# Kernel tuning notes

Hardware: AMD Instinct MI355X
Metric: run time of the kernel (lower is better)

## Reference

```python
import jax, jax.numpy as jnp
import numpy as np

NUM_QUBITS = 21
NUM_LAYERS = 4
ACTION_DIM = 18
STATE_DIM = 2 ** NUM_QUBITS  # amplitude register size


def _rx(t):
    c = jnp.cos(t / 2)
    s = jnp.sin(t / 2)
    return jnp.stack([jnp.stack([c + 0j, -1j * s]), jnp.stack([-1j * s, c + 0j])]).astype(jnp.complex64)


def _ry(t):
    c = jnp.cos(t / 2)
    s = jnp.sin(t / 2)
    return jnp.stack([jnp.stack([c, -s]), jnp.stack([s, c])]).astype(jnp.complex64)


def _rz(t):
    e = jnp.exp(-1j * t / 2).astype(jnp.complex64)
    z = jnp.zeros_like(e)
    return jnp.stack([jnp.stack([e, z]), jnp.stack([z, jnp.conj(e)])])


def apply_1q(psi, U, q):
    # wire 0 is the most-significant bit (PennyLane convention)
    s = psi.reshape(2 ** q, 2, -1)
    s = jnp.einsum('ab,xbz->xaz', U, s)
    return s.reshape(-1)


def apply_cnot(psi, c, t):
    a, b = (c, t) if c < t else (t, c)
    s = psi.reshape(2 ** a, 2, 2 ** (b - a - 1), 2, -1)
    ctrl_ax = 1 if c < t else 3
    tgt_ax = 3 if c < t else 1
    s0 = jax.lax.index_in_dim(s, 0, axis=ctrl_ax, keepdims=False)
    s1 = jax.lax.index_in_dim(s, 1, axis=ctrl_ax, keepdims=False)
    tgt_in_slab = tgt_ax if tgt_ax < ctrl_ax else tgt_ax - 1
    s1 = jnp.flip(s1, axis=tgt_in_slab)  # X on target where control==1
    s = jnp.stack([s0, s1], axis=ctrl_ax)
    return s.reshape(-1)


def _layer(psi, lp, entangle):
    # lp: (NUM_QUBITS, 3) rotation angles for this layer
    for q in range(NUM_QUBITS):
        psi = apply_1q(psi, _rx(lp[q, 0]), q)
        psi = apply_1q(psi, _ry(lp[q, 1]), q)
        psi = apply_1q(psi, _rz(lp[q, 2]), q)
    if entangle:
        for q in range(NUM_QUBITS - 1):
            psi = apply_cnot(psi, q, q + 1)
        psi = apply_cnot(psi, NUM_QUBITS - 1, 0)
    return psi


def setup_inputs() -> dict:
    key = jax.random.key(0)
    k1, k2, k3, k4 = jax.random.split(key, 4)
    state = jax.random.normal(k1, (STATE_DIM,), dtype=jnp.float32)
    circuit_params = jax.random.normal(k2, (NUM_LAYERS * NUM_QUBITS * 3,), dtype=jnp.float32) * 0.01
    bound = 1.0 / np.sqrt(NUM_QUBITS)
    head_w = jax.random.uniform(k3, (ACTION_DIM, NUM_QUBITS), jnp.float32, -bound, bound)
    head_b = jax.random.uniform(k4, (ACTION_DIM,), jnp.float32, -bound, bound)
    return {'state': state, 'circuit_params': circuit_params, 'head_w': head_w, 'head_b': head_b}


def reference(state, circuit_params, head_w, head_b):
    # Amplitude encoding: normalize (state_dim == 2**num_qubits so no padding needed)
    norm = jnp.linalg.norm(state)
    inv = jnp.where(norm > 0, 1.0 / jnp.maximum(norm, 1e-30), 0.0)
    basis0 = jnp.zeros((STATE_DIM,), jnp.float32).at[0].set(1.0)
    amp = jnp.where(norm > 0, state * inv, basis0)
    psi = amp.astype(jnp.complex64)

    lp = circuit_params.reshape(NUM_LAYERS, NUM_QUBITS, 3)
    for layer in range(NUM_LAYERS):
        psi = _layer(psi, lp[layer], layer < NUM_LAYERS - 1)

    # Pauli-Z expectation values per qubit from |psi|^2
    probs = psi.real ** 2 + psi.imag ** 2
    zvals = []
    for q in range(NUM_QUBITS):
        p = probs.reshape(2 ** q, 2, -1)
        zvals.append(p[:, 0, :].sum() - p[:, 1, :].sum())
    meas = jnp.stack(zvals).astype(jnp.float32)

    logits = head_w @ meas + head_b
    return jax.nn.softmax(logits, axis=-1)
```

## Files before the change

### kernel.cpp

```cpp
#include <hip/hip_runtime.h>

#define NQ 21
#define DIM (1 << NQ)
#define NL 4
#define ADIM 18
#define GB 512
#define NT 512

__device__ __forceinline__ float2 cfma2(float2 u0, float2 a, float2 u1, float2 b) {
    return make_float2(u0.x * a.x - u0.y * a.y + u1.x * b.x - u1.y * b.y,
                       u0.x * a.y + u0.y * a.x + u1.x * b.y + u1.y * b.x);
}

struct GateU { float2 u00, u01, u10, u11; };

__device__ __forceinline__ void bfly(float2& a, float2& b, const GateU& U) {
    float2 na = cfma2(U.u00, a, U.u01, b);
    float2 nb = cfma2(U.u10, a, U.u11, b);
    a = na; b = nb;
}

__device__ __forceinline__ int sw(int j) { return j ^ (((j >> 4) & 7) << 1); }

__device__ __forceinline__ void make_mats(GateU* mats, const float* __restrict__ cp, int layer, int tid) {
    if (tid < NQ) {
        const float* ang = cp + (layer * NQ + tid) * 3;
        float a = ang[0], b = ang[1], c = ang[2];
        float ca = cosf(0.5f * a), sa = sinf(0.5f * a);
        float cb = cosf(0.5f * b), sb = sinf(0.5f * b);
        float cc = cosf(0.5f * c), sc = sinf(0.5f * c);
        float2 m00 = make_float2(cb * ca,  sb * sa);
        float2 m01 = make_float2(-sb * ca, -cb * sa);
        float2 m10 = make_float2(sb * ca,  -cb * sa);
        float2 m11 = make_float2(cb * ca,  -sb * sa);
        GateU U;
        U.u00 = make_float2(cc * m00.x + sc * m00.y, cc * m00.y - sc * m00.x);
        U.u01 = make_float2(cc * m01.x + sc * m01.y, cc * m01.y - sc * m01.x);
        U.u10 = make_float2(cc * m10.x - sc * m10.y, cc * m10.y + sc * m10.x);
        U.u11 = make_float2(cc * m11.x - sc * m11.y, cc * m11.y + sc * m11.x);
        mats[tid] = U;
    }
}

__device__ __forceinline__ void round3(float2* tile, int tid, int g,
                                       GateU Ua, GateU Ub, GateU Uc) {
    int bl = (1 << g) - 1;
    int base = (tid & bl) | ((tid >> g) << (g + 3));
    float2 v[8];
#pragma unroll
    for (int j = 0; j < 8; ++j) v[j] = tile[sw(base + (j << g))];
#pragma unroll
    for (int s = 0; s < 8; s += 2) bfly(v[s], v[s + 1], Ua);
#pragma unroll
    for (int s = 0; s < 8; ++s) if (!(s & 2)) bfly(v[s], v[s | 2], Ub);
#pragma unroll
    for (int s = 0; s < 8; ++s) if (!(s & 4)) bfly(v[s], v[s | 4], Uc);
#pragma unroll
    for (int j = 0; j < 8; ++j) tile[sw(base + (j << g))] = v[j];
    __syncthreads();
}

__global__ __launch_bounds__(NT, 4) void k_passB(const float* __restrict__ state,
                                                 float2* __restrict__ psi,
                                                 const float* __restrict__ cp, int layer) {
    __shared__ float2 tile[4096];
    __shared__ GateU mats[NQ];
    const int tid = threadIdx.x, blk = blockIdx.x;
    float4* psi4 = (float4*)psi;
    float4* t4 = (float4*)tile;

    if (layer == 0) {
        const float4* s4 = (const float4*)state;
        for (int it = 0; it < 2; ++it) {
            int f2 = it * NT + tid;
            int h = f2 >> 1, c2 = f2 & 1;
            float4 w = s4[(h << 10) | (blk << 1) | c2];
            int j = 8 * h + 4 * c2;
            t4[sw(j) >> 1]     = make_float4(w.x, 0.f, w.y, 0.f);
            t4[sw(j + 2) >> 1] = make_float4(w.z, 0.f, w.w, 0.f);
        }
        make_mats(mats, cp, layer, tid);
        __syncthreads();
        round3(tile, tid, 3, mats[8], mats[7], mats[6]);
        round3(tile, tid, 6, mats[5], mats[4], mats[3]);
        round3(tile, tid, 9, mats[2], mats[1], mats[0]);
    } else {
        float2 v[8];
        float4 w[4];
        for (int i = 0; i < 4; ++i) {
            int f = i * NT + tid;
            int h = f >> 2, c = f & 3;
            w[i] = psi4[(h << 11) | (blk << 2) | c];
        }
        make_mats(mats, cp, layer, tid);
        __syncthreads();
#pragma unroll
        for (int i = 0; i < 4; ++i) {
            v[2 * i]     = make_float2(w[i].x, w[i].y);
            v[2 * i + 1] = make_float2(w[i ^ 2].z, w[i ^ 2].w);
        }
        GateU U0 = mats[0];
#pragma unroll
        for (int s = 0; s < 8; ++s) if (!(s & 4)) bfly(v[s], v[s | 4], U0);
        GateU U1 = mats[1];
#pragma unroll
        for (int s = 0; s < 8; ++s) if (!(s & 2)) bfly(v[s], v[s | 2], U1);
        for (int i = 0; i < 4; ++i)
            t4[sw(2 * (i * NT + tid)) >> 1] =
                make_float4(v[2 * i].x, v[2 * i].y, v[2 * i + 1].x, v[2 * i + 1].y);
        __syncthreads();
        round3(tile, tid, 3, mats[8], mats[7], mats[6]);
        round3(tile, tid, 6, mats[5], mats[4], mats[3]);
        {
            GateU U = mats[2];
            for (int it = 0; it < 4; ++it) {
                int p = it * NT + tid;
                int i0 = ((p >> 9) << 10) | (p & 511);
                bfly(tile[sw(i0)], tile[sw(i0 | 512)], U);
            }
            __syncthreads();
        }
    }
    int srcmask = (layer < 3) ? 0xFF : 0;
    for (int i = 0; i < 4; ++i) {
        int f = i * NT + tid;
        int h = f >> 2, c = f & 3;
        int hs = h ^ ((h >> 1) & srcmask);
        int j = sw(hs * 8 + 2 * c);
        float2 e0 = tile[j], e1 = tile[j + 1];
        psi4[(h << 11) | (blk << 2) | c] = make_float4(e0.x, e0.y, e1.x, e1.y);
    }
}

__global__ __launch_bounds__(NT, 4) void k_passA(float2* __restrict__ psi,
                                                 const float* __restrict__ cp, int layer,
                                                 float* __restrict__ partials) {
    __shared__ float2 tile[4096];
    __shared__ GateU mats[NQ];
    const int tid = threadIdx.x, blk = blockIdx.x;
    float4* psi4 = (float4*)psi;
    float4* t4 = (float4*)tile;

    {
        const float4* ga = psi4 + (size_t)blk * 2048;
        float2 v[8];
        float4 w[4];
        for (int i = 0; i < 4; ++i) w[i] = ga[i * NT + tid];
        make_mats(mats, cp, layer, tid);
        __syncthreads();
#pragma unroll
        for (int i = 0; i < 4; ++i) {
            v[2 * i]     = make_float2(w[i].x, w[i].y);
            v[2 * i + 1] = make_float2(w[i].z, w[i].w);
        }
        GateU U20 = mats[20];
#pragma unroll
        for (int s = 0; s < 8; s += 2) bfly(v[s], v[s + 1], U20);
        GateU U10 = mats[10];
#pragma unroll
        for (int s = 0; s < 8; ++s) if (!(s & 2)) bfly(v[s], v[s | 2], U10);
        GateU U9 = mats[9];
#pragma unroll
        for (int s = 0; s < 8; ++s) if (!(s & 4)) bfly(v[s], v[s | 4], U9);
        for (int i = 0; i < 4; ++i)
            t4[sw(2 * (i * NT + tid)) >> 1] =
                make_float4(v[2 * i].x, v[2 * i].y, v[2 * i + 1].x, v[2 * i + 1].y);
    }
    __syncthreads();
    round3(tile, tid, 1, mats[19], mats[18], mats[17]);
    round3(tile, tid, 4, mats[16], mats[15], mats[14]);
    round3(tile, tid, 7, mats[13], mats[12], mats[11]);

    if (layer < 3) {
        float4* oa = psi4 + (size_t)blk * 2048;
        int cb = (blk & 1) << 11;
        for (int i = 0; i < 4; ++i) {
            int f = i * NT + tid;
            int s0 = ((2 * f) ^ (f & 0x7FF)) ^ cb;
            float2 e0 = tile[sw(s0)], e1 = tile[sw(s0 ^ 1)];
            oa[f] = make_float4(e0.x, e0.y, e1.x, e1.y);
        }
    } else {
        float tot = 0.f, ones[NQ];
#pragma unroll
        for (int q = 0; q < NQ; ++q) ones[q] = 0.f;
        for (int it = 0; it < 8; ++it) {
            int j = it * NT + tid;
            float2 a2 = tile[sw(j)];
            float pr = a2.x * a2.x + a2.y * a2.y;
            int gidx = (blk << 12) | j;
            tot += pr;
#pragma unroll
            for (int q = 0; q < NQ; ++q)
                ones[q] += pr * (float)((gidx >> (20 - q)) & 1);
        }
        for (int off = 32; off; off >>= 1) {
            tot += __shfl_down(tot, off, 64);
#pragma unroll
            for (int q = 0; q < NQ; ++q) ones[q] += __shfl_down(ones[q], off, 64);
        }
        __syncthreads();
        float* red = (float*)tile;
        int wv = tid >> 6, ln = tid & 63;
        if (ln == 0) {
            red[wv * 22 + 21] = tot;
#pragma unroll
            for (int q = 0; q < NQ; ++q) red[wv * 22 + q] = ones[q];
        }
        __syncthreads();
        if (tid < 22) {
            float s = 0.f;
            for (int wvi = 0; wvi < 8; ++wvi) s += red[wvi * 22 + tid];
            partials[blk * 22 + tid] = s;
        }
    }
}

__global__ __launch_bounds__(NT) void k_final(const float* __restrict__ partials,
                                              const float* __restrict__ head_w,
                                              const float* __restrict__ head_b,
                                              float* __restrict__ out) {
    __shared__ float red[640];
    __shared__ float meas[NQ];
    __shared__ float lg[ADIM];
    int tid = threadIdx.x;
    int col = tid % 22, grp = tid / 22;
    if (tid < 506) {
        float s = 0.f;
        for (int r = grp; r < GB; r += 23) s += partials[r * 22 + col];
        red[grp * 22 + col] = s;
    }
    __syncthreads();
    if (tid < 22) {
        float t2 = 0.f;
        for (int g = 0; g < 23; ++g) t2 += red[g * 22 + tid];
        red[600 + tid] = t2;
    }
    __syncthreads();
    if (tid < NQ) {
        float tot = red[600 + 21];
        meas[tid] = (tot > 0.f) ? (1.f - 2.f * red[600 + tid] / tot) : 1.f;
    }
    __syncthreads();
    if (tid < ADIM) {
        float s2 = head_b[tid];
        for (int q = 0; q < NQ; ++q) s2 += head_w[tid * NQ + q] * meas[q];
        lg[tid] = s2;
    }
    __syncthreads();
    if (tid == 0) {
        float m = lg[0];
        for (int a = 1; a < ADIM; ++a) m = fmaxf(m, lg[a]);
        float ssum = 0.f;
        for (int a = 0; a < ADIM; ++a) ssum += expf(lg[a] - m);
        float inv = 1.f / ssum;
        for (int a = 0; a < ADIM; ++a) out[a] = expf(lg[a] - m) * inv;
    }
}

extern "C" void kernel_launch(void* const* d_in, const int* in_sizes, int n_in,
                              void* d_out, int out_size, void* d_ws, size_t ws_size,
                              hipStream_t stream) {
    const float* state   = (const float*)d_in[0];
    const float* cparams = (const float*)d_in[1];
    const float* head_w  = (const float*)d_in[2];
    const float* head_b  = (const float*)d_in[3];
    float* out = (float*)d_out;

    float2* psi      = (float2*)d_ws;
    float*  partials = (float*)((char*)d_ws + (size_t)DIM * 8);

    for (int layer = 0; layer < NL; ++layer) {
        k_passB<<<GB, NT, 0, stream>>>(state, psi, cparams, layer);
        k_passA<<<GB, NT, 0, stream>>>(psi, cparams, layer, partials);
    }
    k_final<<<1, NT, 0, stream>>>(partials, head_w, head_b, out);
}
```

Baseline: 207.9 us.

## Fuse all layer passes into one persistent kernel with grid barriers

Replaces the nine separate kernel launches (two passes per layer plus the final reduction) with a single persistent kernel of 512 blocks. The blocks synchronise through a software grid barrier built on striped atomic counters and a flag polled by block 0. Global memory traffic uses cache-bypassing sc0 sc1 loads and stores so data is coherent across blocks. The aim is to remove per-launch overhead and tail gaps between passes, at the cost of barrier spin latency, a memset launch, and a deadlock risk if all 512 blocks cannot be co-resident.

```diff
diff --git a/kernel.cpp b/kernel.cpp
--- a/kernel.cpp
+++ b/kernel.cpp
@@ -7,6 +7,8 @@
 #define GB 512
 #define NT 512
 
+typedef float vf4 __attribute__((ext_vector_type(4)));
+
 __device__ __forceinline__ float2 cfma2(float2 u0, float2 a, float2 u1, float2 b) {
     return make_float2(u0.x * a.x - u0.y * a.y + u1.x * b.x - u1.y * b.y,
                        u0.x * a.y + u0.y * a.x + u1.x * b.y + u1.y * b.x);
@@ -21,6 +23,77 @@
 }
 
 __device__ __forceinline__ int sw(int j) { return j ^ (((j >> 4) & 7) << 1); }
+
+__device__ __forceinline__ void load4x16_sc(const float* p0, const float* p1,
+                                            const float* p2, const float* p3,
+                                            vf4& w0, vf4& w1, vf4& w2, vf4& w3) {
+    asm volatile(
+        "global_load_dwordx4 %0, %4, off sc0 sc1\n\t"
+        "global_load_dwordx4 %1, %5, off sc0 sc1\n\t"
+        "global_load_dwordx4 %2, %6, off sc0 sc1\n\t"
+        "global_load_dwordx4 %3, %7, off sc0 sc1\n\t"
+        "s_waitcnt vmcnt(0)"
+        : "=&v"(w0), "=&v"(w1), "=&v"(w2), "=&v"(w3)
+        : "v"(p0), "v"(p1), "v"(p2), "v"(p3)
+        : "memory");
+}
+__device__ __forceinline__ void store16_sc(float* p, vf4 v) {
+    asm volatile("global_store_dwordx4 %0, %1, off sc0 sc1" :: "v"(p), "v"(v) : "memory");
+}
+__device__ __forceinline__ void store4_sc(float* p, float v) {
+    asm volatile("global_store_dword %0, %1, off sc0 sc1" :: "v"(p), "v"(v) : "memory");
+}
+__device__ __forceinline__ void store4i_sc(int* p, int v) {
+    asm volatile("global_store_dword %0, %1, off sc0 sc1" :: "v"(p), "v"(v) : "memory");
+}
+__device__ __forceinline__ int load_sc_i(const int* p) {
+    int r;
+    asm volatile("global_load_dword %0, %1, off sc0 sc1\n\ts_waitcnt vmcnt(0)"
+                 : "=v"(r) : "v"(p) : "memory");
+    return r;
+}
+__device__ __forceinline__ void load4x4_sc(const float* p0, const float* p1,
+                                           const float* p2, const float* p3,
+                                           float& a, float& b, float& c, float& d) {
+    asm volatile(
+        "global_load_dword %0, %4, off sc0 sc1\n\t"
+        "global_load_dword %1, %5, off sc0 sc1\n\t"
+        "global_load_dword %2, %6, off sc0 sc1\n\t"
+        "global_load_dword %3, %7, off sc0 sc1\n\t"
+        "s_waitcnt vmcnt(0)"
+        : "=&v"(a), "=&v"(b), "=&v"(c), "=&v"(d)
+        : "v"(p0), "v"(p1), "v"(p2), "v"(p3)
+        : "memory");
+}
+__device__ __forceinline__ void drain_vmem() {
+    asm volatile("s_waitcnt vmcnt(0)" ::: "memory");
+}
+
+__device__ __forceinline__ void gbar(int* cnt, int* flag, int phase, int tid, int blk) {
+    drain_vmem();
+    __syncthreads();
+    if (tid == 0) atomicAdd(&cnt[(blk & 63) << 5], 1);
+    if (blk == 0) {
+        if (tid < 64) {
+            const int target = (phase + 1) * GB;
+            while (true) {
+                int vv = load_sc_i(&cnt[tid << 5]);
+                for (int o = 32; o; o >>= 1) vv += __shfl_down(vv, o, 64);
+                vv = __shfl(vv, 0, 64);
+                if (vv >= target) break;
+                __builtin_amdgcn_s_sleep(8);
+            }
+            if (tid == 0) store4i_sc(flag, phase + 1);
+        }
+        __syncthreads();
+    } else {
+        if (tid == 0) {
+            const int target = phase + 1;
+            while (load_sc_i(flag) < target) __builtin_amdgcn_s_sleep(8);
+        }
+        __syncthreads();
+    }
+}
 
 __device__ __forceinline__ void make_mats(GateU* mats, const float* __restrict__ cp, int layer, int tid) {
     if (tid < NQ) {
@@ -60,201 +133,227 @@
     __syncthreads();
 }
 
-__global__ __launch_bounds__(NT, 4) void k_passB(const float* __restrict__ state,
-                                                 float2* __restrict__ psi,
-                                                 const float* __restrict__ cp, int layer) {
+__global__ __launch_bounds__(NT, 4) void qpn_kernel(
+    const float* __restrict__ state, const float* __restrict__ cp,
+    const float* __restrict__ head_w, const float* __restrict__ head_b,
+    float* __restrict__ out, float2* __restrict__ psi,
+    float* __restrict__ partials, int* __restrict__ cnt, int* __restrict__ flag)
+{
     __shared__ float2 tile[4096];
     __shared__ GateU mats[NQ];
-    const int tid = threadIdx.x, blk = blockIdx.x;
-    float4* psi4 = (float4*)psi;
-    float4* t4 = (float4*)tile;
-
-    if (layer == 0) {
-        const float4* s4 = (const float4*)state;
-        for (int it = 0; it < 2; ++it) {
-            int f2 = it * NT + tid;
-            int h = f2 >> 1, c2 = f2 & 1;
-            float4 w = s4[(h << 10) | (blk << 1) | c2];
-            int j = 8 * h + 4 * c2;
-            t4[sw(j) >> 1]     = make_float4(w.x, 0.f, w.y, 0.f);
-            t4[sw(j + 2) >> 1] = make_float4(w.z, 0.f, w.w, 0.f);
-        }
-        make_mats(mats, cp, layer, tid);
-        __syncthreads();
-        round3(tile, tid, 3, mats[8], mats[7], mats[6]);
-        round3(tile, tid, 6, mats[5], mats[4], mats[3]);
-        round3(tile, tid, 9, mats[2], mats[1], mats[0]);
-    } else {
-        float2 v[8];
-        float4 w[4];
-        for (int i = 0; i < 4; ++i) {
-            int f = i * NT + tid;
-            int h = f >> 2, c = f & 3;
-            w[i] = psi4[(h << 11) | (blk << 2) | c];
-        }
-        make_mats(mats, cp, layer, tid);
-        __syncthreads();
-#pragma unroll
-        for (int i = 0; i < 4; ++i) {
-            v[2 * i]     = make_float2(w[i].x, w[i].y);
-            v[2 * i + 1] = make_float2(w[i ^ 2].z, w[i ^ 2].w);
-        }
-        GateU U0 = mats[0];
-#pragma unroll
-        for (int s = 0; s < 8; ++s) if (!(s & 4)) bfly(v[s], v[s | 4], U0);
-        GateU U1 = mats[1];
-#pragma unroll
-        for (int s = 0; s < 8; ++s) if (!(s & 2)) bfly(v[s], v[s | 2], U1);
-        for (int i = 0; i < 4; ++i)
-            t4[sw(2 * (i * NT + tid)) >> 1] =
-                make_float4(v[2 * i].x, v[2 * i].y, v[2 * i + 1].x, v[2 * i + 1].y);
-        __syncthreads();
-        round3(tile, tid, 3, mats[8], mats[7], mats[6]);
-        round3(tile, tid, 6, mats[5], mats[4], mats[3]);
-        {
-            GateU U = mats[2];
-            for (int it = 0; it < 4; ++it) {
-                int p = it * NT + tid;
-                int i0 = ((p >> 9) << 10) | (p & 511);
-                bfly(tile[sw(i0)], tile[sw(i0 | 512)], U);
-            }
-            __syncthreads();
-        }
-    }
-    int srcmask = (layer < 3) ? 0xFF : 0;
-    for (int i = 0; i < 4; ++i) {
-        int f = i * NT + tid;
-        int h = f >> 2, c = f & 3;
-        int hs = h ^ ((h >> 1) & srcmask);
-        int j = sw(hs * 8 + 2 * c);
-        float2 e0 = tile[j], e1 = tile[j + 1];
-        psi4[(h << 11) | (blk << 2) | c] = make_float4(e0.x, e0.y, e1.x, e1.y);
-    }
-}
-
-__global__ __launch_bounds__(NT, 4) void k_passA(float2* __restrict__ psi,
-                                                 const float* __restrict__ cp, int layer,
-                                                 float* __restrict__ partials) {
-    __shared__ float2 tile[4096];
-    __shared__ GateU mats[NQ];
-    const int tid = threadIdx.x, blk = blockIdx.x;
-    float4* psi4 = (float4*)psi;
-    float4* t4 = (float4*)tile;
-
-    {
-        const float4* ga = psi4 + (size_t)blk * 2048;
-        float2 v[8];
-        float4 w[4];
-        for (int i = 0; i < 4; ++i) w[i] = ga[i * NT + tid];
-        make_mats(mats, cp, layer, tid);
-        __syncthreads();
-#pragma unroll
-        for (int i = 0; i < 4; ++i) {
-            v[2 * i]     = make_float2(w[i].x, w[i].y);
-            v[2 * i + 1] = make_float2(w[i].z, w[i].w);
-        }
-        GateU U20 = mats[20];
-#pragma unroll
-        for (int s = 0; s < 8; s += 2) bfly(v[s], v[s + 1], U20);
-        GateU U10 = mats[10];
-#pragma unroll
-        for (int s = 0; s < 8; ++s) if (!(s & 2)) bfly(v[s], v[s | 2], U10);
-        GateU U9 = mats[9];
-#pragma unroll
-        for (int s = 0; s < 8; ++s) if (!(s & 4)) bfly(v[s], v[s | 4], U9);
-        for (int i = 0; i < 4; ++i)
-            t4[sw(2 * (i * NT + tid)) >> 1] =
-                make_float4(v[2 * i].x, v[2 * i].y, v[2 * i + 1].x, v[2 * i + 1].y);
-    }
-    __syncthreads();
-    round3(tile, tid, 1, mats[19], mats[18], mats[17]);
-    round3(tile, tid, 4, mats[16], mats[15], mats[14]);
-    round3(tile, tid, 7, mats[13], mats[12], mats[11]);
-
-    if (layer < 3) {
-        float4* oa = psi4 + (size_t)blk * 2048;
-        int cb = (blk & 1) << 11;
-        for (int i = 0; i < 4; ++i) {
-            int f = i * NT + tid;
-            int s0 = ((2 * f) ^ (f & 0x7FF)) ^ cb;
-            float2 e0 = tile[sw(s0)], e1 = tile[sw(s0 ^ 1)];
-            oa[f] = make_float4(e0.x, e0.y, e1.x, e1.y);
-        }
-    } else {
-        float tot = 0.f, ones[NQ];
-#pragma unroll
-        for (int q = 0; q < NQ; ++q) ones[q] = 0.f;
-        for (int it = 0; it < 8; ++it) {
-            int j = it * NT + tid;
-            float2 a2 = tile[sw(j)];
-            float pr = a2.x * a2.x + a2.y * a2.y;
-            int gidx = (blk << 12) | j;
-            tot += pr;
-#pragma unroll
-            for (int q = 0; q < NQ; ++q)
-                ones[q] += pr * (float)((gidx >> (20 - q)) & 1);
-        }
-        for (int off = 32; off; off >>= 1) {
-            tot += __shfl_down(tot, off, 64);
-#pragma unroll
-            for (int q = 0; q < NQ; ++q) ones[q] += __shfl_down(ones[q], off, 64);
-        }
-        __syncthreads();
-        float* red = (float*)tile;
-        int wv = tid >> 6, ln = tid & 63;
-        if (ln == 0) {
-            red[wv * 22 + 21] = tot;
-#pragma unroll
-            for (int q = 0; q < NQ; ++q) red[wv * 22 + q] = ones[q];
-        }
-        __syncthreads();
-        if (tid < 22) {
-            float s = 0.f;
-            for (int wvi = 0; wvi < 8; ++wvi) s += red[wvi * 22 + tid];
-            partials[blk * 22 + tid] = s;
-        }
-    }
-}
-
-__global__ __launch_bounds__(NT) void k_final(const float* __restrict__ partials,
-                                              const float* __restrict__ head_w,
-                                              const float* __restrict__ head_b,
-                                              float* __restrict__ out) {
-    __shared__ float red[640];
     __shared__ float meas[NQ];
     __shared__ float lg[ADIM];
-    int tid = threadIdx.x;
-    int col = tid % 22, grp = tid / 22;
-    if (tid < 506) {
-        float s = 0.f;
-        for (int r = grp; r < GB; r += 23) s += partials[r * 22 + col];
-        red[grp * 22 + col] = s;
+    const int tid = threadIdx.x, blk = blockIdx.x;
+    float* psif = (float*)psi;
+    float4* t4 = (float4*)tile;
+
+    for (int layer = 0; layer < NL; ++layer) {
+        if (layer == 0) {
+            const float4* s4 = (const float4*)state;
+            for (int it = 0; it < 2; ++it) {
+                int f2 = it * NT + tid;
+                int h = f2 >> 1, c2 = f2 & 1;
+                float4 w = s4[(h << 10) | (blk << 1) | c2];
+                int j = 8 * h + 4 * c2;
+                t4[sw(j) >> 1]     = make_float4(w.x, 0.f, w.y, 0.f);
+                t4[sw(j + 2) >> 1] = make_float4(w.z, 0.f, w.w, 0.f);
+            }
+            make_mats(mats, cp, layer, tid);
+            __syncthreads();
+            round3(tile, tid, 3, mats[8], mats[7], mats[6]);
+            round3(tile, tid, 6, mats[5], mats[4], mats[3]);
+            round3(tile, tid, 9, mats[2], mats[1], mats[0]);
+        } else {
+            float2 v[8];
+            vf4 w[4];
+            {
+                int f0 = tid,          h0 = f0 >> 2, c0 = f0 & 3;
+                int f1 = NT + tid,     h1 = f1 >> 2, c1 = f1 & 3;
+                int f2 = 2 * NT + tid, h2 = f2 >> 2, c2 = f2 & 3;
+                int f3 = 3 * NT + tid, h3 = f3 >> 2, c3 = f3 & 3;
+                load4x16_sc(psif + 4 * (size_t)((h0 << 11) | (blk << 2) | c0),
+                            psif + 4 * (size_t)((h1 << 11) | (blk << 2) | c1),
+                            psif + 4 * (size_t)((h2 << 11) | (blk << 2) | c2),
+                            psif + 4 * (size_t)((h3 << 11) | (blk << 2) | c3),
+                            w[0], w[1], w[2], w[3]);
+            }
+            make_mats(mats, cp, layer, tid);
+            __syncthreads();
+#pragma unroll
+            for (int i = 0; i < 4; ++i) {
+                v[2 * i]     = make_float2(w[i].x, w[i].y);
+                v[2 * i + 1] = make_float2(w[i ^ 2].z, w[i ^ 2].w);
+            }
+            GateU U0 = mats[0];
+#pragma unroll
+            for (int s = 0; s < 8; ++s) if (!(s & 4)) bfly(v[s], v[s | 4], U0);
+            GateU U1 = mats[1];
+#pragma unroll
+            for (int s = 0; s < 8; ++s) if (!(s & 2)) bfly(v[s], v[s | 2], U1);
+            for (int i = 0; i < 4; ++i)
+                t4[sw(2 * (i * NT + tid)) >> 1] =
+                    make_float4(v[2 * i].x, v[2 * i].y, v[2 * i + 1].x, v[2 * i + 1].y);
+            __syncthreads();
+            round3(tile, tid, 3, mats[8], mats[7], mats[6]);
+            round3(tile, tid, 6, mats[5], mats[4], mats[3]);
+            {
+                GateU U = mats[2];
+                for (int it = 0; it < 4; ++it) {
+                    int p = it * NT + tid;
+                    int i0 = ((p >> 9) << 10) | (p & 511);
+                    bfly(tile[sw(i0)], tile[sw(i0 | 512)], U);
+                }
+                __syncthreads();
+            }
+        }
+        {
+            int srcmask = (layer < 3) ? 0xFF : 0;
+            for (int i = 0; i < 4; ++i) {
+                int f = i * NT + tid;
+                int h = f >> 2, c = f & 3;
+                int hs = h ^ ((h >> 1) & srcmask);
+                int j = sw(hs * 8 + 2 * c);
+                float2 e0 = tile[j], e1 = tile[j + 1];
+                vf4 val = {e0.x, e0.y, e1.x, e1.y};
+                store16_sc(psif + 4 * (size_t)((h << 11) | (blk << 2) | c), val);
+            }
+        }
+        gbar(cnt, flag, 2 * layer, tid, blk);
+
+        {
+            float* ga = psif + (size_t)blk * 8192;
+            float2 v[8];
+            vf4 w[4];
+            load4x16_sc(ga + 4 * (size_t)tid, ga + 4 * (size_t)(NT + tid),
+                        ga + 4 * (size_t)(2 * NT + tid), ga + 4 * (size_t)(3 * NT + tid),
+                        w[0], w[1], w[2], w[3]);
+#pragma unroll
+            for (int i = 0; i < 4; ++i) {
+                v[2 * i]     = make_float2(w[i].x, w[i].y);
+                v[2 * i + 1] = make_float2(w[i].z, w[i].w);
+            }
+            GateU U20 = mats[20];
+#pragma unroll
+            for (int s = 0; s < 8; s += 2) bfly(v[s], v[s + 1], U20);
+            GateU U10 = mats[10];
+#pragma unroll
+            for (int s = 0; s < 8; ++s) if (!(s & 2)) bfly(v[s], v[s | 2], U10);
+            GateU U9 = mats[9];
+#pragma unroll
+            for (int s = 0; s < 8; ++s) if (!(s & 4)) bfly(v[s], v[s | 4], U9);
+            for (int i = 0; i < 4; ++i)
+                t4[sw(2 * (i * NT + tid)) >> 1] =
+                    make_float4(v[2 * i].x, v[2 * i].y, v[2 * i + 1].x, v[2 * i + 1].y);
+        }
+        __syncthreads();
+        round3(tile, tid, 1, mats[19], mats[18], mats[17]);
+        round3(tile, tid, 4, mats[16], mats[15], mats[14]);
+        round3(tile, tid, 7, mats[13], mats[12], mats[11]);
+
+        if (layer < 3) {
+            float* oa = psif + (size_t)blk * 8192;
+            int cb = (blk & 1) << 11;
+            for (int i = 0; i < 4; ++i) {
+                int f = i * NT + tid;
+                int s0 = ((2 * f) ^ (f & 0x7FF)) ^ cb;
+                float2 e0 = tile[sw(s0)], e1 = tile[sw(s0 ^ 1)];
+                vf4 val = {e0.x, e0.y, e1.x, e1.y};
+                store16_sc(oa + 4 * (size_t)f, val);
+            }
+            gbar(cnt, flag, 2 * layer + 1, tid, blk);
+        } else {
+            float tot = 0.f, ones[NQ];
+#pragma unroll
+            for (int q = 0; q < NQ; ++q) ones[q] = 0.f;
+            for (int it = 0; it < 8; ++it) {
+                int j = it * NT + tid;
+                float2 a2 = tile[sw(j)];
+                float pr = a2.x * a2.x + a2.y * a2.y;
+                int gidx = (blk << 12) | j;
+                tot += pr;
+#pragma unroll
+                for (int q = 0; q < NQ; ++q)
+                    ones[q] += pr * (float)((gidx >> (20 - q)) & 1);
+            }
+            for (int off = 32; off; off >>= 1) {
+                tot += __shfl_down(tot, off, 64);
+#pragma unroll
+                for (int q = 0; q < NQ; ++q) ones[q] += __shfl_down(ones[q], off, 64);
+            }
+            __syncthreads();
+            float* red = (float*)tile;
+            int wv = tid >> 6, ln = tid & 63;
+            if (ln == 0) {
+                red[wv * 22 + 21] = tot;
+#pragma unroll
+                for (int q = 0; q < NQ; ++q) red[wv * 22 + q] = ones[q];
+            }
+            __syncthreads();
+            if (tid < 22) {
+                float s = 0.f;
+                for (int wvi = 0; wvi < 8; ++wvi) s += red[wvi * 22 + tid];
+                store4_sc(&partials[blk * 22 + tid], s);
+            }
+            drain_vmem();
+            __syncthreads();
+            if (tid == 0) atomicAdd(&cnt[(blk & 63) << 5], 1);
+            if (blk != 0) return;
+            if (tid < 64) {
+                while (true) {
+                    int vv = load_sc_i(&cnt[tid << 5]);
+                    for (int o = 32; o; o >>= 1) vv += __shfl_down(vv, o, 64);
+                    vv = __shfl(vv, 0, 64);
+                    if (vv >= 8 * GB) break;
+                    __builtin_amdgcn_s_sleep(8);
+                }
+            }
+            __syncthreads();
+        }
     }
-    __syncthreads();
-    if (tid < 22) {
-        float t2 = 0.f;
-        for (int g = 0; g < 23; ++g) t2 += red[g * 22 + tid];
-        red[600 + tid] = t2;
-    }
-    __syncthreads();
-    if (tid < NQ) {
-        float tot = red[600 + 21];
-        meas[tid] = (tot > 0.f) ? (1.f - 2.f * red[600 + tid] / tot) : 1.f;
-    }
-    __syncthreads();
-    if (tid < ADIM) {
-        float s2 = head_b[tid];
-        for (int q = 0; q < NQ; ++q) s2 += head_w[tid * NQ + q] * meas[q];
-        lg[tid] = s2;
-    }
-    __syncthreads();
-    if (tid == 0) {
-        float m = lg[0];
-        for (int a = 1; a < ADIM; ++a) m = fmaxf(m, lg[a]);
-        float ssum = 0.f;
-        for (int a = 0; a < ADIM; ++a) ssum += expf(lg[a] - m);
-        float inv = 1.f / ssum;
-        for (int a = 0; a < ADIM; ++a) out[a] = expf(lg[a] - m) * inv;
+
+    {
+        float* red = (float*)tile;
+        int col = tid % 22, grp = tid / 22;
+        if (tid < 506) {
+            float s = 0.f;
+            const float* base = partials + col;
+#pragma unroll
+            for (int kk = 0; kk < 6; ++kk) {
+                int r0 = grp + 92 * kk;
+                float a, b, c, d;
+                load4x4_sc(base + (size_t)r0 * 22, base + (size_t)(r0 + 23) * 22,
+                           base + (size_t)(r0 + 46) * 22, base + (size_t)(r0 + 69) * 22,
+                           a, b, c, d);
+                s += a + b + c + d;
+            }
+            red[grp * 22 + col] = s;
+        }
+        __syncthreads();
+        if (tid < 22) {
+            float t2 = 0.f;
+            for (int g = 0; g < 23; ++g) t2 += red[g * 22 + tid];
+            red[600 + tid] = t2;
+        }
+        __syncthreads();
+        if (tid < NQ) {
+            float tot = red[600 + 21];
+            meas[tid] = (tot > 0.f) ? (1.f - 2.f * red[600 + tid] / tot) : 1.f;
+        }
+        __syncthreads();
+        if (tid < ADIM) {
+            float s2 = head_b[tid];
+            for (int q = 0; q < NQ; ++q) s2 += head_w[tid * NQ + q] * meas[q];
+            lg[tid] = s2;
+        }
+        __syncthreads();
+        if (tid == 0) {
+            float m = lg[0];
+            for (int a = 1; a < ADIM; ++a) m = fmaxf(m, lg[a]);
+            float ssum = 0.f;
+            for (int a = 0; a < ADIM; ++a) ssum += expf(lg[a] - m);
+            float inv = 1.f / ssum;
+            for (int a = 0; a < ADIM; ++a) out[a] = expf(lg[a] - m) * inv;
+        }
     }
 }
 
@@ -267,12 +366,13 @@
     const float* head_b  = (const float*)d_in[3];
     float* out = (float*)d_out;
 
-    float2* psi      = (float2*)d_ws;
-    float*  partials = (float*)((char*)d_ws + (size_t)DIM * 8);
-
-    for (int layer = 0; layer < NL; ++layer) {
-        k_passB<<<GB, NT, 0, stream>>>(state, psi, cparams, layer);
-        k_passA<<<GB, NT, 0, stream>>>(psi, cparams, layer, partials);
-    }
-    k_final<<<1, NT, 0, stream>>>(partials, head_w, head_b, out);
-}
+    char* ws = (char*)d_ws;
+    float2* psi      = (float2*)ws;
+    float*  partials = (float*)(ws + (size_t)DIM * 8);
+    int*    cnt      = (int*)  (ws + (size_t)DIM * 8 + 49152);
+    int*    flag     = (int*)  (ws + (size_t)DIM * 8 + 49152 + 8192);
+
+    hipMemsetAsync(ws + (size_t)DIM * 8, 0, 49152 + 8192 + 128, stream);
+    qpn_kernel<<<GB, NT, 0, stream>>>(state, cparams, head_w, head_b, out,
+                                      psi, partials, cnt, flag);
+}
```

Result: slower. 244.4 us (+17.6%).

## Halve passB grid and process two column halves per block with unified path

Applied to the files above, without the earlier changes.

passB now launches 256 blocks, each looping over two halves of a wider column slab. The layer>0 special path, which applied gates 0 and 1 in registers, is replaced by a single path that folds part of the CNOT permutation into shared-memory index swizzling and runs three round3 stages. The intent is to simplify the code and amortize gate-matrix setup across more work per block. The cost is an extra sync per half, lower grid parallelism, and layer>0 now using shared-memory rounds instead of register butterflies.

```diff
diff --git a/kernel.cpp b/kernel.cpp
--- a/kernel.cpp
+++ b/kernel.cpp
@@ -4,7 +4,8 @@
 #define DIM (1 << NQ)
 #define NL 4
 #define ADIM 18
-#define GB 512
+#define GBA 512
+#define GBB 256
 #define NT 512
 
 __device__ __forceinline__ float2 cfma2(float2 u0, float2 a, float2 u1, float2 b) {
@@ -67,68 +68,46 @@
     __shared__ GateU mats[NQ];
     const int tid = threadIdx.x, blk = blockIdx.x;
     float4* psi4 = (float4*)psi;
-    float4* t4 = (float4*)tile;
-
-    if (layer == 0) {
-        const float4* s4 = (const float4*)state;
-        for (int it = 0; it < 2; ++it) {
-            int f2 = it * NT + tid;
-            int h = f2 >> 1, c2 = f2 & 1;
-            float4 w = s4[(h << 10) | (blk << 1) | c2];
-            int j = 8 * h + 4 * c2;
-            t4[sw(j) >> 1]     = make_float4(w.x, 0.f, w.y, 0.f);
-            t4[sw(j + 2) >> 1] = make_float4(w.z, 0.f, w.w, 0.f);
-        }
-        make_mats(mats, cp, layer, tid);
+
+    make_mats(mats, cp, layer, tid);
+    const int srcmask = (layer < 3) ? 0xFF : 0;
+
+    for (int H = 0; H < 2; ++H) {
+        if (H) __syncthreads();
+        if (layer == 0) {
+            const float4* s4 = (const float4*)state;
+            for (int i = 0; i < 2; ++i) {
+                int f = i * NT + tid;
+                int d = f & 1, h = f >> 1;
+                float4 w = s4[(h << 10) | (blk << 2) | (2 * H + d)];
+                int s = (h << 3) | (4 * d);
+                tile[sw(s)]     = make_float2(w.x, 0.f);
+                tile[sw(s + 1)] = make_float2(w.y, 0.f);
+                tile[sw(s + 2)] = make_float2(w.z, 0.f);
+                tile[sw(s + 3)] = make_float2(w.w, 0.f);
+            }
+        } else {
+            for (int i = 0; i < 4; ++i) {
+                int f = i * NT + tid;
+                int c = f & 3, h = f >> 2;
+                float4 w = psi4[(h << 11) | (blk << 3) | (4 * H + c)];
+                int se = (h << 3) | (2 * c);
+                tile[sw(se)]            = make_float2(w.x, w.y);
+                tile[sw((se + 1) ^ 2048)] = make_float2(w.z, w.w);
+            }
+        }
         __syncthreads();
         round3(tile, tid, 3, mats[8], mats[7], mats[6]);
         round3(tile, tid, 6, mats[5], mats[4], mats[3]);
         round3(tile, tid, 9, mats[2], mats[1], mats[0]);
-    } else {
-        float2 v[8];
-        float4 w[4];
         for (int i = 0; i < 4; ++i) {
             int f = i * NT + tid;
-            int h = f >> 2, c = f & 3;
-            w[i] = psi4[(h << 11) | (blk << 2) | c];
-        }
-        make_mats(mats, cp, layer, tid);
-        __syncthreads();
-#pragma unroll
-        for (int i = 0; i < 4; ++i) {
-            v[2 * i]     = make_float2(w[i].x, w[i].y);
-            v[2 * i + 1] = make_float2(w[i ^ 2].z, w[i ^ 2].w);
-        }
-        GateU U0 = mats[0];
-#pragma unroll
-        for (int s = 0; s < 8; ++s) if (!(s & 4)) bfly(v[s], v[s | 4], U0);
-        GateU U1 = mats[1];
-#pragma unroll
-        for (int s = 0; s < 8; ++s) if (!(s & 2)) bfly(v[s], v[s | 2], U1);
-        for (int i = 0; i < 4; ++i)
-            t4[sw(2 * (i * NT + tid)) >> 1] =
-                make_float4(v[2 * i].x, v[2 * i].y, v[2 * i + 1].x, v[2 * i + 1].y);
-        __syncthreads();
-        round3(tile, tid, 3, mats[8], mats[7], mats[6]);
-        round3(tile, tid, 6, mats[5], mats[4], mats[3]);
-        {
-            GateU U = mats[2];
-            for (int it = 0; it < 4; ++it) {
-                int p = it * NT + tid;
-                int i0 = ((p >> 9) << 10) | (p & 511);
-                bfly(tile[sw(i0)], tile[sw(i0 | 512)], U);
-            }
-            __syncthreads();
-        }
-    }
-    int srcmask = (layer < 3) ? 0xFF : 0;
-    for (int i = 0; i < 4; ++i) {
-        int f = i * NT + tid;
-        int h = f >> 2, c = f & 3;
-        int hs = h ^ ((h >> 1) & srcmask);
-        int j = sw(hs * 8 + 2 * c);
-        float2 e0 = tile[j], e1 = tile[j + 1];
-        psi4[(h << 11) | (blk << 2) | c] = make_float4(e0.x, e0.y, e1.x, e1.y);
+            int c = f & 3, h = f >> 2;
+            int hs = h ^ ((h >> 1) & srcmask);
+            int s = (hs << 3) | (2 * c);
+            float2 e0 = tile[sw(s)], e1 = tile[sw(s + 1)];
+            psi4[(h << 11) | (blk << 3) | (4 * H + c)] = make_float4(e0.x, e0.y, e1.x, e1.y);
+        }
     }
 }
 
@@ -227,7 +206,7 @@
     int col = tid % 22, grp = tid / 22;
     if (tid < 506) {
         float s = 0.f;
-        for (int r = grp; r < GB; r += 23) s += partials[r * 22 + col];
+        for (int r = grp; r < GBA; r += 23) s += partials[r * 22 + col];
         red[grp * 22 + col] = s;
     }
     __syncthreads();
@@ -271,8 +250,8 @@
     float*  partials = (float*)((char*)d_ws + (size_t)DIM * 8);
 
     for (int layer = 0; layer < NL; ++layer) {
-        k_passB<<<GB, NT, 0, stream>>>(state, psi, cparams, layer);
-        k_passA<<<GB, NT, 0, stream>>>(psi, cparams, layer, partials);
+        k_passB<<<GBB, NT, 0, stream>>>(state, psi, cparams, layer);
+        k_passA<<<GBA, NT, 0, stream>>>(psi, cparams, layer, partials);
     }
     k_final<<<1, NT, 0, stream>>>(partials, head_w, head_b, out);
 }
```

Result: slower. 214.9 us (+3.4%).
